# Performance work log

Measured on AMD Instinct MI355X. Metric: run time of the kernel, lower is better.

Reference implementation:

```python
import jax, jax.numpy as jnp
import numpy as np

B, L, D = 8, 2048, 1024


def _hippo(d, seed=0):
    # Author's 'hippo_matrix': Q @ diag(arctan(linspace(0, pi, d))) @ Q.T with Q orthogonal.
    rng = np.random.default_rng(seed)
    Q, _ = np.linalg.qr(rng.standard_normal((d, d)))
    Dm = np.diag(np.arctan(np.linspace(0.0, np.pi, d)))
    return (Q @ Dm @ Q.T).astype(np.float32)


def setup_inputs() -> dict:
    key = jax.random.key(0)
    k1, k2, k3, k4 = jax.random.split(key, 4)
    x = jax.random.normal(k1, (B, L, D), jnp.float32)
    A_w = jnp.asarray(_hippo(D))                                   # [D, D], spectral norm <= arctan(pi)
    C_w = jax.random.normal(k2, (D, D), jnp.float32) * (D ** -0.5)  # readout C
    # rc maps cat(x_t, y_{t-1}, y_container) (3D) -> D; small init keeps the
    # linear recurrence spectral radius < 1 so the 2048-step scan stays finite.
    rc_w = jax.random.normal(k3, (D, 3 * D), jnp.float32) * (0.2 / np.sqrt(3 * D))
    rc_b = jax.random.normal(k4, (D,), jnp.float32) * 0.02
    return {"x": x, "A_w": A_w, "C_w": C_w, "rc_w": rc_w, "rc_b": rc_b}


def reference(x, A_w, C_w, rc_w, rc_b):
    # y[0] = x[0]; y[t] = C @ A @ (rc_w @ cat(x[t], y[t-1], y[t-1]) + rc_b)
    # (prev output enters twice: once via the outer forward_step cat, once via
    #  the LinearRecurrentContainer's internal memory y).
    d = x.shape[-1]
    Wx = rc_w[:, :d]                          # acts on x_t
    Wy = rc_w[:, d:2 * d] + rc_w[:, 2 * d:]   # both copies of y_{t-1}
    M = C_w @ A_w                             # fused C∘A readout, [D, D]
    P = M @ Wx                                # input map
    Q = M @ Wy                                # recurrence map
    c = M @ rc_b                              # fused bias
    u = jnp.einsum('bld,ed->ble', x[:, 1:], P) + c  # driving terms for t >= 1, [B, L-1, D]
    y0 = x[:, 0]                              # parallel_scan copies the first input verbatim

    def step(y_prev, u_t):
        y = u_t + y_prev @ Q.T                # [B, D]
        return y, y

    _, ys = jax.lax.scan(step, y0, jnp.swapaxes(u, 0, 1))  # [L-1, B, D]
    return jnp.concatenate([y0[:, None, :], jnp.swapaxes(ys, 0, 1)], axis=1)  # [B, L, D]
```

## Files before the change

### kernel.cpp

```cpp
#include <hip/hip_runtime.h>

typedef unsigned short u16;
typedef unsigned int   u32;
typedef __attribute__((ext_vector_type(8))) short short8;
typedef __attribute__((ext_vector_type(4))) short short4v;
typedef __attribute__((ext_vector_type(4))) float f32x4;

__device__ __forceinline__ float bf2f(u16 v) {
  u32 x = ((u32)v) << 16;
  return __builtin_bit_cast(float, x);
}
__device__ __forceinline__ u16 f2bf(float f) {
  u32 x = __builtin_bit_cast(u32, f);
  x += 0x7FFFu + ((x >> 16) & 1u);
  return (u16)(x >> 16);
}
__device__ __forceinline__ void gload_lds16(const u16* g, u16* l) {
  __builtin_amdgcn_global_load_lds(
      (const __attribute__((address_space(1))) u32*)g,
      (__attribute__((address_space(3))) u32*)l, 16, 0, 0);
}

template <int BM, int BN, int ADT, int BDT, int EPI, int AMAP, int OMAP,
          int COUT, int TRW, int SQF>
__global__ __launch_bounds__(256) void gemm_nt(
    const void* __restrict__ Av, int lda, const void* __restrict__ Bv, int ldb,
    void* __restrict__ Cv, int ldc, int Mrows, int K,
    const float* __restrict__ zrowF, const u16* __restrict__ zrowB,
    const float* __restrict__ bias, const float* __restrict__ addf,
    float* __restrict__ Yout, u16* __restrict__ aux16, int jp1, int shoff,
    const u16* __restrict__ sqA, const u16* __restrict__ sqB,
    u16* __restrict__ sqC, u16* __restrict__ sqCt) {
  constexpr int WM = BM / 2, WN = BN / 2;
  constexpr int MT = WM / 16, NTT = WN / 16;
  constexpr int AIn = ADT ? BM * 8 : BM * 4;
  constexpr int BIn = BDT ? BN * 8 : BN * 4;
  static_assert(AIn >= 256 && BIn >= 256, "tile too small for 256 threads");
  constexpr int AI = AIn / 256, BI = BIn / 256;
  __shared__ u16 lA[BM * 32];
  __shared__ u16 lB[BN * 32];
  const int tid = threadIdx.x;
  const int lane = tid & 63, wid = tid >> 6;
  const int wm = wid & 1, wn = wid >> 1;
  const bool role = (SQF == 1) && ((int)blockIdx.x >= 32);
  const int bxe = role ? ((int)blockIdx.x - 32) : (int)blockIdx.x;
  const int m0 = bxe * BM, n0 = blockIdx.y * BN;
  const int effM = role ? 1024 : Mrows;
  const int q = lane >> 4, lm = lane & 15;
  const int cq = (q ^ (lm & 3)) * 8;

  f32x4 acc[MT][NTT];
#pragma unroll
  for (int mi = 0; mi < MT; ++mi)
#pragma unroll
    for (int ni = 0; ni < NTT; ++ni) acc[mi][ni] = (f32x4){0.f, 0.f, 0.f, 0.f};

  const u16* aB[AI];
  const float* aF[AI];
#pragma unroll
  for (int i = 0; i < AI; ++i) {
    int g = tid + i * 256;
    int r = ADT ? (g >> 3) : (g >> 2);
    int c = ADT ? (g & 7) : (g & 3);
    int row = m0 + r;
    bool valid = (row < effM);
    if (AMAP == 1 && !role) {
      int p = row % 257;
      if (p < shoff) valid = false;
      row -= shoff;
    }
    if constexpr (ADT == 1) {
      int cs = ((((c >> 1) ^ (r & 3)) << 1) | (c & 1)) * 4;
      aF[i] = (valid ? (const float*)Av + (long)row * lda : zrowF) + cs;
    } else {
      int cs = (c ^ (r & 3)) * 8;
      const u16* base =
          role ? sqA + (long)row * 1024
               : (valid ? (const u16*)Av + (long)row * lda : zrowB);
      if (!role && !valid) base = zrowB;
      aB[i] = base + cs;
    }
  }
  const u16* bB[BI];
  const float* bF[BI];
#pragma unroll
  for (int i = 0; i < BI; ++i) {
    int g = tid + i * 256;
    int r = BDT ? (g >> 3) : (g >> 2);
    int c = BDT ? (g & 7) : (g & 3);
    if constexpr (BDT == 1) {
      int cs = ((((c >> 1) ^ (r & 3)) << 1) | (c & 1)) * 4;
      bF[i] = (const float*)Bv + (long)(n0 + r) * ldb + cs;
    } else {
      int cs = (c ^ (r & 3)) * 8;
      const u16* base = role ? sqB + (long)(n0 + r) * 1024
                             : (const u16*)Bv + (long)(n0 + r) * ldb;
      bB[i] = base + cs;
    }
  }

  for (int k0 = 0; k0 < K; k0 += 32) {
    f32x4 fa[AI], fb[BI];
    if constexpr (ADT == 1) {
#pragma unroll
      for (int i = 0; i < AI; ++i) fa[i] = *(const f32x4*)(aF[i] + k0);
    }
    if constexpr (BDT == 1) {
#pragma unroll
      for (int i = 0; i < BI; ++i) fb[i] = *(const f32x4*)(bF[i] + k0);
    }
    __syncthreads();
    if constexpr (ADT == 0) {
#pragma unroll
      for (int i = 0; i < AI; ++i)
        gload_lds16(aB[i] + k0, &lA[(tid + i * 256) * 8]);
    } else {
#pragma unroll
      for (int i = 0; i < AI; ++i) {
        short4v s = {(short)f2bf(fa[i][0]), (short)f2bf(fa[i][1]),
                     (short)f2bf(fa[i][2]), (short)f2bf(fa[i][3])};
        *(short4v*)&lA[(tid + i * 256) * 4] = s;
      }
    }
    if constexpr (BDT == 0) {
#pragma unroll
      for (int i = 0; i < BI; ++i)
        gload_lds16(bB[i] + k0, &lB[(tid + i * 256) * 8]);
    } else {
#pragma unroll
      for (int i = 0; i < BI; ++i) {
        short4v s = {(short)f2bf(fb[i][0]), (short)f2bf(fb[i][1]),
                     (short)f2bf(fb[i][2]), (short)f2bf(fb[i][3])};
        *(short4v*)&lB[(tid + i * 256) * 4] = s;
      }
    }
    __syncthreads();
    short8 af[MT], bf[NTT];
#pragma unroll
    for (int mi = 0; mi < MT; ++mi)
      af[mi] = *(const short8*)&lA[(wm * WM + mi * 16 + lm) * 32 + cq];
#pragma unroll
    for (int ni = 0; ni < NTT; ++ni)
      bf[ni] = *(const short8*)&lB[(wn * WN + ni * 16 + lm) * 32 + cq];
#pragma unroll
    for (int mi = 0; mi < MT; ++mi)
#pragma unroll
      for (int ni = 0; ni < NTT; ++ni)
        acc[mi][ni] = __builtin_amdgcn_mfma_f32_16x16x32_bf16(
            af[mi], bf[ni], acc[mi][ni], 0, 0, 0);
  }

#pragma unroll
  for (int mi = 0; mi < MT; ++mi) {
    int rbase = m0 + wm * WM + mi * 16 + q * 4;
#pragma unroll
    for (int ni = 0; ni < NTT; ++ni) {
      int ocol = n0 + wn * WN + ni * 16 + lm;
#pragma unroll
      for (int r = 0; r < 4; ++r) {
        int orow = rbase + r;
        float v = acc[mi][ni][r];
        if (role) {
          if (orow < 1024) {
            u16 ov = f2bf(v);
            sqC[(long)orow * 1024 + ocol] = ov;
            sqCt[(long)ocol * 1024 + orow] = ov;
          }
          continue;
        }
        if (orow >= Mrows) continue;
        if constexpr (EPI == 5) {
          v += bias[ocol];
          bool isT0 = (orow & 2047) == 0;
          if (isT0) v = addf[(long)orow * 1024 + ocol];
          ((float*)Cv)[(long)orow * ldc + ocol] = v;
          if (isT0) Yout[((long)(orow >> 11) * 257) * 1024 + ocol] = v;
          if ((orow & 7) == 1)
            aux16[((long)(orow >> 3)) * 1024 + ocol] = f2bf(v);
          continue;
        }
        if constexpr (EPI == 6) {
          v += addf[(long)orow * 1024 + ocol];
          ((float*)Cv)[(long)orow * ldc + ocol] = v;
          int b = orow / 257;
          int pp_ = orow - b * 257;
          if (pp_ < 256)
            aux16[((long)(b * 256 + pp_)) * 1024 + ocol] = f2bf(v);
          continue;
        }
        long urow = 0;
        bool uok = true;
        if constexpr (EPI == 2 || EPI == 3) {
          urow = 8L * orow + jp1;
          uok = ((urow & 2047) != 0);
          if (uok) v += addf[urow * 1024 + ocol];
        }
        if constexpr (EPI == 4) v += addf[(long)orow * 1024 + ocol];
        long wrow = orow;
        if constexpr (OMAP == 1)
          wrow = (long)(orow >> 8) * 257 + (orow & 255) + 1;
        if constexpr (COUT == 1)
          ((float*)Cv)[wrow * (long)ldc + ocol] = v;
        else
          ((u16*)Cv)[wrow * (long)ldc + ocol] = f2bf(v);
        if constexpr (TRW == 1) aux16[(long)ocol * ldc + orow] = f2bf(v);
        if constexpr (EPI == 3) {
          if (uok) Yout[urow * 1024 + ocol] = v;
        }
      }
    }
  }
}

__global__ void zero_misc(float* zF, u16* zB) {
  for (int i = threadIdx.x; i < 2048; i += 256) {
    zF[i] = 0.f;
    zB[i] = 0;
  }
}
__global__ void xconv(const float* __restrict__ x, u16* __restrict__ xb) {
  long i = (long)blockIdx.x * 256 + threadIdx.x;
  f32x4 v = ((const f32x4*)x)[i];
  short4v s = {(short)f2bf(v[0]), (short)f2bf(v[1]), (short)f2bf(v[2]),
               (short)f2bf(v[3])};
  ((short4v*)xb)[i] = s;
}
__global__ void prep_wt(const float* __restrict__ rc_w, u16* __restrict__ WxT,
                        u16* __restrict__ WyT) {
  __shared__ u16 tx[64][65];
  __shared__ u16 ty[64][65];
  int kb = blockIdx.x * 64, db = blockIdx.y * 64;
  for (int i = threadIdx.x; i < 64 * 64; i += 256) {
    int r = i >> 6, c = i & 63;
    long base = (long)(kb + r) * 3072 + db + c;
    tx[r][c] = f2bf(rc_w[base]);
    ty[r][c] = f2bf(rc_w[base + 1024] + rc_w[base + 2048]);
  }
  __syncthreads();
  for (int i = threadIdx.x; i < 64 * 64; i += 256) {
    int r = i >> 6, c = i & 63;
    WxT[(long)(db + r) * 1024 + kb + c] = tx[c][r];
    WyT[(long)(db + r) * 1024 + kb + c] = ty[c][r];
  }
}
__global__ void matvec_c(const u16* __restrict__ M_,
                         const float* __restrict__ rb,
                         float* __restrict__ cvec) {
  int row = blockIdx.x;
  int lane = threadIdx.x;
  float s = 0.f;
  for (int k = lane; k < 1024; k += 64)
    s += bf2f(M_[(long)row * 1024 + k]) * rb[k];
  for (int o = 32; o > 0; o >>= 1) s += __shfl_down(s, o, 64);
  if (lane == 0) cvec[row] = s;
}

extern "C" void kernel_launch(void* const* d_in, const int* in_sizes, int n_in,
                              void* d_out, int out_size, void* d_ws,
                              size_t ws_size, hipStream_t stream) {
  const float* x = (const float*)d_in[0];
  const float* A_w = (const float*)d_in[1];
  const float* C_w = (const float*)d_in[2];
  const float* rc_w = (const float*)d_in[3];
  const float* rc_b = (const float*)d_in[4];
  float* Y = (float*)d_out;

  char* ws = (char*)d_ws;
  const long MB = 1 << 20;
  u16* Z0 = (u16*)(ws);
  u16* Z1 = (u16*)(ws + 4 * MB);
  float* Bnd0 = (float*)(ws + 8 * MB);
  float* Bnd1 = (float*)(ws + 8 * MB + 8912896);
  char* p = ws + 25 * MB;
  u16* Mbuf = (u16*)p;
  u16* WxT = (u16*)(p + 2 * MB);
  u16* WyT = (u16*)(p + 4 * MB);
  u16* Pbuf = (u16*)(p + 6 * MB);
  u16* Qbuf = (u16*)(p + 8 * MB);
  u16* QbufT = (u16*)(p + 10 * MB);
  float* cvec = (float*)(p + 12 * MB);
  float* zF = (float*)(p + 12 * MB + 4096);
  u16* zB = (u16*)(p + 12 * MB + 12288);
  u16* xbf = (u16*)(p + 12 * MB + 16384);
  const size_t need_fast = (size_t)(25 * MB + 12 * MB + 16384) + 33554432;
  const bool fast = ws_size >= need_fast;

  dim3 blk(256);
  zero_misc<<<dim3(1), blk, 0, stream>>>(zF, zB);
  if (fast) xconv<<<dim3(16384), blk, 0, stream>>>(x, xbf);
  prep_wt<<<dim3(16, 16), blk, 0, stream>>>(rc_w, WxT, WyT);

  gemm_nt<64, 64, 1, 1, 0, 0, 0, 0, 0, 0><<<dim3(16, 16), blk, 0, stream>>>(
      C_w, 1024, A_w, 1024, Mbuf, 1024, 1024, 1024, zF, zB, nullptr, nullptr,
      nullptr, nullptr, 0, 0, nullptr, nullptr, nullptr, nullptr);
  gemm_nt<64, 64, 0, 0, 0, 0, 0, 0, 0, 0><<<dim3(16, 16), blk, 0, stream>>>(
      Mbuf, 1024, WxT, 1024, Pbuf, 1024, 1024, 1024, zF, zB, nullptr, nullptr,
      nullptr, nullptr, 0, 0, nullptr, nullptr, nullptr, nullptr);
  gemm_nt<64, 64, 0, 0, 0, 0, 0, 0, 1, 0><<<dim3(16, 16), blk, 0, stream>>>(
      Mbuf, 1024, WyT, 1024, Qbuf, 1024, 1024, 1024, zF, zB, nullptr, nullptr,
      nullptr, QbufT, 0, 0, nullptr, nullptr, nullptr, nullptr);
  matvec_c<<<dim3(1024), dim3(64), 0, stream>>>(Mbuf, rc_b, cvec);

  if (fast)
    gemm_nt<128, 128, 0, 0, 5, 0, 0, 1, 0, 0>
        <<<dim3(128, 8), blk, 0, stream>>>(xbf, 1024, Pbuf, 1024, Y, 1024,
                                           16384, 1024, zF, zB, cvec, x, Bnd0,
                                           Z0, 0, 0, nullptr, nullptr, nullptr,
                                           nullptr);
  else
    gemm_nt<128, 128, 1, 0, 5, 0, 0, 1, 0, 0>
        <<<dim3(128, 8), blk, 0, stream>>>(x, 1024, Pbuf, 1024, Y, 1024, 16384,
                                           1024, zF, zB, cvec, x, Bnd0, Z0, 0,
                                           0, nullptr, nullptr, nullptr,
                                           nullptr);

  u16* Tb[7];
  u16* Tt[7];
  if (fast) {
    for (int i = 0; i < 7; ++i) {
      Tb[i] = xbf + (long)i * 2097152;
      Tt[i] = Tb[i] + 1048576;
    }
  } else {
    for (int i = 0; i < 7; ++i) {
      Tb[i] = (i & 1) ? Mbuf : WxT;
      Tt[i] = (i & 1) ? Pbuf : WyT;
    }
  }

  for (int j = 1; j <= 6; ++j) {
    const u16* zin = (j & 1) ? Z0 : Z1;
    u16* zout = (j & 1) ? Z1 : Z0;
    const u16* si = (j == 1) ? Qbuf : Tb[j - 2];
    const u16* st = (j == 1) ? QbufT : Tt[j - 2];
    if (fast)
      gemm_nt<64, 64, 0, 0, 2, 0, 0, 0, 0, 1>
          <<<dim3(48, 16), blk, 0, stream>>>(zin, 1024, Qbuf, 1024, zout, 1024,
                                             2048, 1024, zF, zB, nullptr, Y,
                                             nullptr, nullptr, j + 1, 0, si,
                                             st, Tb[j - 1], Tt[j - 1]);
    else
      gemm_nt<64, 64, 0, 0, 2, 0, 0, 0, 0, 0>
          <<<dim3(32, 16), blk, 0, stream>>>(zin, 1024, Qbuf, 1024, zout, 1024,
                                             2048, 1024, zF, zB, nullptr, Y,
                                             nullptr, nullptr, j + 1, 0,
                                             nullptr, nullptr, nullptr,
                                             nullptr);
  }
  if (fast)
    gemm_nt<64, 64, 0, 0, 2, 0, 1, 1, 0, 1><<<dim3(48, 16), blk, 0, stream>>>(
        Z0, 1024, Qbuf, 1024, Bnd0, 1024, 2048, 1024, zF, zB, nullptr, Y,
        nullptr, nullptr, 8, 0, Tb[5], Tt[5], Tb[6], Tt[6]);
  else
    gemm_nt<64, 64, 0, 0, 2, 0, 1, 1, 0, 0><<<dim3(32, 16), blk, 0, stream>>>(
        Z0, 1024, Qbuf, 1024, Bnd0, 1024, 2048, 1024, zF, zB, nullptr, Y,
        nullptr, nullptr, 8, 0, nullptr, nullptr, nullptr, nullptr);

  if (!fast) {
    for (int i = 0; i < 3; ++i) {
      const u16* si = (i == 0) ? Qbuf : Tb[i - 1];
      const u16* st = (i == 0) ? QbufT : Tt[i - 1];
      gemm_nt<64, 64, 0, 0, 0, 0, 0, 0, 1, 0>
          <<<dim3(16, 16), blk, 0, stream>>>(si, 1024, st, 1024, Tb[i], 1024,
                                             1024, 1024, zF, zB, nullptr,
                                             nullptr, nullptr, Tt[i], 0, 0,
                                             nullptr, nullptr, nullptr,
                                             nullptr);
    }
  }

  float* bc = Bnd0;
  float* bn = Bnd1;
  for (int s = 0; s < 5; ++s) {
    if (s < 4)
      gemm_nt<64, 64, 1, 0, 4, 1, 0, 1, 0, 0>
          <<<dim3(33, 16), blk, 0, stream>>>(bc, 1024, Tb[s + 2], 1024, bn,
                                             1024, 2056, 1024, zF, zB, nullptr,
                                             bc, nullptr, nullptr, 0, 1 << s,
                                             nullptr, nullptr, nullptr,
                                             nullptr);
    else
      gemm_nt<64, 64, 1, 0, 6, 1, 0, 1, 0, 0>
          <<<dim3(33, 16), blk, 0, stream>>>(bc, 1024, Tb[s + 2], 1024, bn,
                                             1024, 2056, 1024, zF, zB, nullptr,
                                             bc, nullptr, Z0, 0, 1 << s,
                                             nullptr, nullptr, nullptr,
                                             nullptr);
    if (!fast && s < 4) {
      int i = s + 3;
      gemm_nt<64, 64, 0, 0, 0, 0, 0, 0, 1, 0>
          <<<dim3(16, 16), blk, 0, stream>>>(Tb[i - 1], 1024, Tt[i - 1], 1024,
                                             Tb[i], 1024, 1024, 1024, zF, zB,
                                             nullptr, nullptr, nullptr, Tt[i],
                                             0, 0, nullptr, nullptr, nullptr,
                                             nullptr);
    }
    float* t = bc;
    bc = bn;
    bn = t;
  }

  for (int j = 0; j <= 7; ++j) {
    const u16* zin = (j & 1) ? Z1 : Z0;
    u16* zout = (j & 1) ? Z0 : Z1;
    gemm_nt<64, 64, 0, 0, 3, 0, 0, 0, 0, 0><<<dim3(32, 16), blk, 0, stream>>>(
        zin, 1024, Qbuf, 1024, zout, 1024, 2048, 1024, zF, zB, nullptr, Y, Y,
        nullptr, j + 1, 0, nullptr, nullptr, nullptr, nullptr);
  }
}
```

Before: 728.3 us.

## Replace final serial correction GEMM chain with one batched power-of-Q kernel

In the fast path, the eight sequential per-offset correction GEMMs at the end are replaced by one launch over a z-grid of 7. Each z-slice multiplies the boundary states by a precomputed power Q^1..Q^7 and writes Y directly. To build those powers, the square-job side blocks now take a struct of up to four independent GEMM jobs per launch, and the Q^2..Q^7 products are spread over the early scan steps. This removes a dependent chain of launches in exchange for more extra-block work per early launch and more bf16 powers of Q, which could add rounding error.

```diff
diff --git a/kernel.cpp b/kernel.cpp
--- a/kernel.cpp
+++ b/kernel.cpp
@@ -5,6 +5,13 @@
 typedef __attribute__((ext_vector_type(8))) short short8;
 typedef __attribute__((ext_vector_type(4))) short short4v;
 typedef __attribute__((ext_vector_type(4))) float f32x4;
+
+struct SqJobs {
+  const u16* a[4];
+  const u16* b[4];
+  u16* c[4];
+  u16* ct[4];
+};
 
 __device__ __forceinline__ float bf2f(u16 v) {
   u32 x = ((u32)v) << 16;
@@ -29,8 +36,7 @@
     const float* __restrict__ zrowF, const u16* __restrict__ zrowB,
     const float* __restrict__ bias, const float* __restrict__ addf,
     float* __restrict__ Yout, u16* __restrict__ aux16, int jp1, int shoff,
-    const u16* __restrict__ sqA, const u16* __restrict__ sqB,
-    u16* __restrict__ sqC, u16* __restrict__ sqCt) {
+    SqJobs jb) {
   constexpr int WM = BM / 2, WN = BN / 2;
   constexpr int MT = WM / 16, NTT = WN / 16;
   constexpr int AIn = ADT ? BM * 8 : BM * 4;
@@ -43,11 +49,18 @@
   const int lane = tid & 63, wid = tid >> 6;
   const int wm = wid & 1, wn = wid >> 1;
   const bool role = (SQF == 1) && ((int)blockIdx.x >= 32);
-  const int bxe = role ? ((int)blockIdx.x - 32) : (int)blockIdx.x;
+  const int pi = role ? (((int)blockIdx.x - 32) >> 4) : 0;
+  const int bxe = role ? (((int)blockIdx.x - 32) & 15) : (int)blockIdx.x;
   const int m0 = bxe * BM, n0 = blockIdx.y * BN;
   const int effM = role ? 1024 : Mrows;
   const int q = lane >> 4, lm = lane & 15;
   const int cq = (q ^ (lm & 3)) * 8;
+
+  const u16* corrB = nullptr;
+  if constexpr (EPI == 7)
+    corrB = (blockIdx.z == 0)
+                ? (const u16*)Bv
+                : jb.a[0] + (long)((int)blockIdx.z - 1) * 1048576;
 
   f32x4 acc[MT][NTT];
 #pragma unroll
@@ -74,10 +87,11 @@
       aF[i] = (valid ? (const float*)Av + (long)row * lda : zrowF) + cs;
     } else {
       int cs = (c ^ (r & 3)) * 8;
-      const u16* base =
-          role ? sqA + (long)row * 1024
-               : (valid ? (const u16*)Av + (long)row * lda : zrowB);
-      if (!role && !valid) base = zrowB;
+      const u16* base;
+      if (role)
+        base = jb.a[pi] + (long)row * 1024;
+      else
+        base = valid ? (const u16*)Av + (long)row * lda : zrowB;
       aB[i] = base + cs;
     }
   }
@@ -93,8 +107,15 @@
       bF[i] = (const float*)Bv + (long)(n0 + r) * ldb + cs;
     } else {
       int cs = (c ^ (r & 3)) * 8;
-      const u16* base = role ? sqB + (long)(n0 + r) * 1024
-                             : (const u16*)Bv + (long)(n0 + r) * ldb;
+      const u16* base;
+      if (role) {
+        base = jb.b[pi] + (long)(n0 + r) * 1024;
+      } else {
+        if constexpr (EPI == 7)
+          base = corrB + (long)(n0 + r) * ldb;
+        else
+          base = (const u16*)Bv + (long)(n0 + r) * ldb;
+      }
       bB[i] = base + cs;
     }
   }
@@ -163,12 +184,18 @@
         if (role) {
           if (orow < 1024) {
             u16 ov = f2bf(v);
-            sqC[(long)orow * 1024 + ocol] = ov;
-            sqCt[(long)ocol * 1024 + orow] = ov;
+            jb.c[pi][(long)orow * 1024 + ocol] = ov;
+            if (jb.ct[pi]) jb.ct[pi][(long)ocol * 1024 + orow] = ov;
           }
           continue;
         }
         if (orow >= Mrows) continue;
+        if constexpr (EPI == 7) {
+          long urow = 8L * orow + ((int)blockIdx.z + 1);
+          float vv = v + addf[urow * 1024 + ocol];
+          Yout[urow * 1024 + ocol] = vv;
+          continue;
+        }
         if constexpr (EPI == 5) {
           v += bias[ocol];
           bool isT0 = (orow & 2047) == 0;
@@ -186,6 +213,8 @@
           int pp_ = orow - b * 257;
           if (pp_ < 256)
             aux16[((long)(b * 256 + pp_)) * 1024 + ocol] = f2bf(v);
+          if (pp_ >= 1 && pp_ < 256)
+            Yout[((long)b * 2048 + 8L * pp_) * 1024 + ocol] = v;
           continue;
         }
         long urow = 0;
@@ -285,6 +314,7 @@
   const size_t need_fast = (size_t)(25 * MB + 12 * MB + 16384) + 33554432;
   const bool fast = ws_size >= need_fast;
 
+  SqJobs J0{};
   dim3 blk(256);
   zero_misc<<<dim3(1), blk, 0, stream>>>(zF, zB);
   if (fast) xconv<<<dim3(16384), blk, 0, stream>>>(x, xbf);
@@ -292,71 +322,120 @@
 
   gemm_nt<64, 64, 1, 1, 0, 0, 0, 0, 0, 0><<<dim3(16, 16), blk, 0, stream>>>(
       C_w, 1024, A_w, 1024, Mbuf, 1024, 1024, 1024, zF, zB, nullptr, nullptr,
-      nullptr, nullptr, 0, 0, nullptr, nullptr, nullptr, nullptr);
+      nullptr, nullptr, 0, 0, J0);
   gemm_nt<64, 64, 0, 0, 0, 0, 0, 0, 0, 0><<<dim3(16, 16), blk, 0, stream>>>(
       Mbuf, 1024, WxT, 1024, Pbuf, 1024, 1024, 1024, zF, zB, nullptr, nullptr,
-      nullptr, nullptr, 0, 0, nullptr, nullptr, nullptr, nullptr);
+      nullptr, nullptr, 0, 0, J0);
   gemm_nt<64, 64, 0, 0, 0, 0, 0, 0, 1, 0><<<dim3(16, 16), blk, 0, stream>>>(
       Mbuf, 1024, WyT, 1024, Qbuf, 1024, 1024, 1024, zF, zB, nullptr, nullptr,
-      nullptr, QbufT, 0, 0, nullptr, nullptr, nullptr, nullptr);
+      nullptr, QbufT, 0, 0, J0);
   matvec_c<<<dim3(1024), dim3(64), 0, stream>>>(Mbuf, rc_b, cvec);
 
   if (fast)
     gemm_nt<128, 128, 0, 0, 5, 0, 0, 1, 0, 0>
         <<<dim3(128, 8), blk, 0, stream>>>(xbf, 1024, Pbuf, 1024, Y, 1024,
                                            16384, 1024, zF, zB, cvec, x, Bnd0,
-                                           Z0, 0, 0, nullptr, nullptr, nullptr,
-                                           nullptr);
+                                           Z0, 0, 0, J0);
   else
     gemm_nt<128, 128, 1, 0, 5, 0, 0, 1, 0, 0>
         <<<dim3(128, 8), blk, 0, stream>>>(x, 1024, Pbuf, 1024, Y, 1024, 16384,
                                            1024, zF, zB, cvec, x, Bnd0, Z0, 0,
-                                           0, nullptr, nullptr, nullptr,
-                                           nullptr);
-
-  u16* Tb[7];
-  u16* Tt[7];
+                                           0, J0);
+
   if (fast) {
-    for (int i = 0; i < 7; ++i) {
-      Tb[i] = xbf + (long)i * 2097152;
-      Tt[i] = Tb[i] + 1048576;
-    }
+    const long M1 = 1048576;
+    u16* PW = xbf;
+    u16* Q2 = PW + 0 * M1;
+    u16* Q3 = PW + 1 * M1;
+    u16* Q4 = PW + 2 * M1;
+    u16* Q5 = PW + 3 * M1;
+    u16* Q6 = PW + 4 * M1;
+    u16* Q7 = PW + 5 * M1;
+    u16* Tb2 = xbf + 6 * M1;
+    u16* Tt2 = xbf + 7 * M1;
+    u16* Tb3 = xbf + 8 * M1;
+    u16* Tt3 = xbf + 9 * M1;
+    u16* Tb4 = xbf + 10 * M1;
+    u16* Tt4 = xbf + 11 * M1;
+    u16* Tb5 = xbf + 12 * M1;
+    u16* Tt5 = xbf + 13 * M1;
+    u16* Tb6 = xbf + 14 * M1;
+    u16* Tt6 = xbf + 15 * M1;
+    u16* Tt0 = Mbuf;
+    u16* Tt1 = WxT;
+    u16* Pw3T = WyT;
+
+    SqJobs sj[7] = {};
+    int nsq[7] = {1, 2, 4, 1, 1, 1, 1};
+    sj[0].a[0] = Qbuf;  sj[0].b[0] = QbufT; sj[0].c[0] = Q2;  sj[0].ct[0] = Tt0;
+    sj[1].a[0] = Q2;    sj[1].b[0] = Tt0;   sj[1].c[0] = Q4;  sj[1].ct[0] = Tt1;
+    sj[1].a[1] = Q2;    sj[1].b[1] = QbufT; sj[1].c[1] = Q3;  sj[1].ct[1] = Pw3T;
+    sj[2].a[0] = Q4;    sj[2].b[0] = Tt1;   sj[2].c[0] = Tb2; sj[2].ct[0] = Tt2;
+    sj[2].a[1] = Q4;    sj[2].b[1] = QbufT; sj[2].c[1] = Q5;
+    sj[2].a[2] = Q4;    sj[2].b[2] = Tt0;   sj[2].c[2] = Q6;
+    sj[2].a[3] = Q4;    sj[2].b[3] = Pw3T;  sj[2].c[3] = Q7;
+    sj[3].a[0] = Tb2;   sj[3].b[0] = Tt2;   sj[3].c[0] = Tb3; sj[3].ct[0] = Tt3;
+    sj[4].a[0] = Tb3;   sj[4].b[0] = Tt3;   sj[4].c[0] = Tb4; sj[4].ct[0] = Tt4;
+    sj[5].a[0] = Tb4;   sj[5].b[0] = Tt4;   sj[5].c[0] = Tb5; sj[5].ct[0] = Tt5;
+    sj[6].a[0] = Tb5;   sj[6].b[0] = Tt5;   sj[6].c[0] = Tb6; sj[6].ct[0] = Tt6;
+
+    for (int j = 1; j <= 6; ++j) {
+      const u16* zin = (j & 1) ? Z0 : Z1;
+      u16* zout = (j & 1) ? Z1 : Z0;
+      gemm_nt<64, 64, 0, 0, 3, 0, 0, 0, 0, 1>
+          <<<dim3(32 + 16 * nsq[j - 1], 16), blk, 0, stream>>>(
+              zin, 1024, Qbuf, 1024, zout, 1024, 2048, 1024, zF, zB, nullptr,
+              Y, Y, nullptr, j + 1, 0, sj[j - 1]);
+    }
+    gemm_nt<64, 64, 0, 0, 2, 0, 1, 1, 0, 1><<<dim3(48, 16), blk, 0, stream>>>(
+        Z0, 1024, Qbuf, 1024, Bnd0, 1024, 2048, 1024, zF, zB, nullptr, Y,
+        nullptr, nullptr, 8, 0, sj[6]);
+
+    u16* TbP2[5] = {Tb2, Tb3, Tb4, Tb5, Tb6};
+    float* bc = Bnd0;
+    float* bn = Bnd1;
+    for (int s = 0; s < 5; ++s) {
+      if (s < 4)
+        gemm_nt<64, 64, 1, 0, 4, 1, 0, 1, 0, 0>
+            <<<dim3(33, 16), blk, 0, stream>>>(bc, 1024, TbP2[s], 1024, bn,
+                                               1024, 2056, 1024, zF, zB,
+                                               nullptr, bc, nullptr, nullptr,
+                                               0, 1 << s, J0);
+      else
+        gemm_nt<64, 64, 1, 0, 6, 1, 0, 1, 0, 0>
+            <<<dim3(33, 16), blk, 0, stream>>>(bc, 1024, TbP2[s], 1024, bn,
+                                               1024, 2056, 1024, zF, zB,
+                                               nullptr, bc, Y, Z0, 0, 1 << s,
+                                               J0);
+      float* t = bc;
+      bc = bn;
+      bn = t;
+    }
+
+    SqJobs cj{};
+    cj.a[0] = PW;
+    gemm_nt<64, 64, 0, 0, 7, 0, 0, 0, 0, 0>
+        <<<dim3(32, 16, 7), blk, 0, stream>>>(Z0, 1024, Qbuf, 1024, Z1, 1024,
+                                              2048, 1024, zF, zB, nullptr, Y,
+                                              Y, nullptr, 0, 0, cj);
   } else {
+    u16* Tb[7];
+    u16* Tt[7];
     for (int i = 0; i < 7; ++i) {
       Tb[i] = (i & 1) ? Mbuf : WxT;
       Tt[i] = (i & 1) ? Pbuf : WyT;
     }
-  }
-
-  for (int j = 1; j <= 6; ++j) {
-    const u16* zin = (j & 1) ? Z0 : Z1;
-    u16* zout = (j & 1) ? Z1 : Z0;
-    const u16* si = (j == 1) ? Qbuf : Tb[j - 2];
-    const u16* st = (j == 1) ? QbufT : Tt[j - 2];
-    if (fast)
-      gemm_nt<64, 64, 0, 0, 2, 0, 0, 0, 0, 1>
-          <<<dim3(48, 16), blk, 0, stream>>>(zin, 1024, Qbuf, 1024, zout, 1024,
-                                             2048, 1024, zF, zB, nullptr, Y,
-                                             nullptr, nullptr, j + 1, 0, si,
-                                             st, Tb[j - 1], Tt[j - 1]);
-    else
+    for (int j = 1; j <= 6; ++j) {
+      const u16* zin = (j & 1) ? Z0 : Z1;
+      u16* zout = (j & 1) ? Z1 : Z0;
       gemm_nt<64, 64, 0, 0, 2, 0, 0, 0, 0, 0>
           <<<dim3(32, 16), blk, 0, stream>>>(zin, 1024, Qbuf, 1024, zout, 1024,
                                              2048, 1024, zF, zB, nullptr, Y,
-                                             nullptr, nullptr, j + 1, 0,
-                                             nullptr, nullptr, nullptr,
-                                             nullptr);
-  }
-  if (fast)
-    gemm_nt<64, 64, 0, 0, 2, 0, 1, 1, 0, 1><<<dim3(48, 16), blk, 0, stream>>>(
-        Z0, 1024, Qbuf, 1024, Bnd0, 1024, 2048, 1024, zF, zB, nullptr, Y,
-        nullptr, nullptr, 8, 0, Tb[5], Tt[5], Tb[6], Tt[6]);
-  else
+                                             nullptr, nullptr, j + 1, 0, J0);
+    }
     gemm_nt<64, 64, 0, 0, 2, 0, 1, 1, 0, 0><<<dim3(32, 16), blk, 0, stream>>>(
         Z0, 1024, Qbuf, 1024, Bnd0, 1024, 2048, 1024, zF, zB, nullptr, Y,
-        nullptr, nullptr, 8, 0, nullptr, nullptr, nullptr, nullptr);
-
-  if (!fast) {
+        nullptr, nullptr, 8, 0, J0);
     for (int i = 0; i < 3; ++i) {
       const u16* si = (i == 0) ? Qbuf : Tb[i - 1];
       const u16* st = (i == 0) ? QbufT : Tt[i - 1];
@@ -364,47 +443,42 @@
           <<<dim3(16, 16), blk, 0, stream>>>(si, 1024, st, 1024, Tb[i], 1024,
                                              1024, 1024, zF, zB, nullptr,
                                              nullptr, nullptr, Tt[i], 0, 0,
-                                             nullptr, nullptr, nullptr,
-                                             nullptr);
-    }
-  }
-
-  float* bc = Bnd0;
-  float* bn = Bnd1;
-  for (int s = 0; s < 5; ++s) {
-    if (s < 4)
-      gemm_nt<64, 64, 1, 0, 4, 1, 0, 1, 0, 0>
-          <<<dim3(33, 16), blk, 0, stream>>>(bc, 1024, Tb[s + 2], 1024, bn,
-                                             1024, 2056, 1024, zF, zB, nullptr,
-                                             bc, nullptr, nullptr, 0, 1 << s,
-                                             nullptr, nullptr, nullptr,
-                                             nullptr);
-    else
-      gemm_nt<64, 64, 1, 0, 6, 1, 0, 1, 0, 0>
-          <<<dim3(33, 16), blk, 0, stream>>>(bc, 1024, Tb[s + 2], 1024, bn,
-                                             1024, 2056, 1024, zF, zB, nullptr,
-                                             bc, nullptr, Z0, 0, 1 << s,
-                                             nullptr, nullptr, nullptr,
-                                             nullptr);
-    if (!fast && s < 4) {
-      int i = s + 3;
-      gemm_nt<64, 64, 0, 0, 0, 0, 0, 0, 1, 0>
-          <<<dim3(16, 16), blk, 0, stream>>>(Tb[i - 1], 1024, Tt[i - 1], 1024,
-                                             Tb[i], 1024, 1024, 1024, zF, zB,
-                                             nullptr, nullptr, nullptr, Tt[i],
-                                             0, 0, nullptr, nullptr, nullptr,
-                                             nullptr);
-    }
-    float* t = bc;
-    bc = bn;
-    bn = t;
-  }
-
-  for (int j = 0; j <= 7; ++j) {
-    const u16* zin = (j & 1) ? Z1 : Z0;
-    u16* zout = (j & 1) ? Z0 : Z1;
-    gemm_nt<64, 64, 0, 0, 3, 0, 0, 0, 0, 0><<<dim3(32, 16), blk, 0, stream>>>(
-        zin, 1024, Qbuf, 1024, zout, 1024, 2048, 1024, zF, zB, nullptr, Y, Y,
-        nullptr, j + 1, 0, nullptr, nullptr, nullptr, nullptr);
-  }
-}
+                                             J0);
+    }
+    float* bc = Bnd0;
+    float* bn = Bnd1;
+    for (int s = 0; s < 5; ++s) {
+      if (s < 4)
+        gemm_nt<64, 64, 1, 0, 4, 1, 0, 1, 0, 0>
+            <<<dim3(33, 16), blk, 0, stream>>>(bc, 1024, Tb[s + 2], 1024, bn,
+                                               1024, 2056, 1024, zF, zB,
+                                               nullptr, bc, nullptr, nullptr,
+                                               0, 1 << s, J0);
+      else
+        gemm_nt<64, 64, 1, 0, 6, 1, 0, 1, 0, 0>
+            <<<dim3(33, 16), blk, 0, stream>>>(bc, 1024, Tb[s + 2], 1024, bn,
+                                               1024, 2056, 1024, zF, zB,
+                                               nullptr, bc, Y, Z0, 0, 1 << s,
+                                               J0);
+      if (s < 4) {
+        int i = s + 3;
+        gemm_nt<64, 64, 0, 0, 0, 0, 0, 0, 1, 0>
+            <<<dim3(16, 16), blk, 0, stream>>>(Tb[i - 1], 1024, Tt[i - 1],
+                                               1024, Tb[i], 1024, 1024, 1024,
+                                               zF, zB, nullptr, nullptr,
+                                               nullptr, Tt[i], 0, 0, J0);
+      }
+      float* t = bc;
+      bc = bn;
+      bn = t;
+    }
+    for (int j = 0; j <= 7; ++j) {
+      const u16* zin = (j & 1) ? Z1 : Z0;
+      u16* zout = (j & 1) ? Z0 : Z1;
+      gemm_nt<64, 64, 0, 0, 3, 0, 0, 0, 0, 0>
+          <<<dim3(32, 16), blk, 0, stream>>>(zin, 1024, Qbuf, 1024, zout, 1024,
+                                             2048, 1024, zF, zB, nullptr, Y, Y,
+                                             nullptr, j + 1, 0, J0);
+    }
+  }
+}
```

Result: faster. 660.3 us (-9.3%).
